# Optimization experiments

Hardware: AMD Instinct MI355X
Metric: run time of the kernel (lower is better)

Reference implementation:

```python
import jax, jax.numpy as jnp
import numpy as np
from jax import lax

NPOINT = 2048
RADIUS = 0.1
NSAMPLE = 32


def setup_inputs() -> dict:
    key = jax.random.key(0)
    ks = jax.random.split(key, 6)
    B, N, C = 8, 16384, 16
    xyz = jax.random.uniform(ks[0], (B, N, 3), dtype=jnp.float32)
    features = jax.random.normal(ks[1], (B, N, C), dtype=jnp.float32)
    W1 = jax.random.normal(ks[2], (C, 32), dtype=jnp.float32) * 0.1
    b1 = jnp.zeros((32,), jnp.float32)
    W2 = jax.random.normal(ks[3], (32, 32), dtype=jnp.float32) * 0.1
    b2 = jnp.zeros((32,), jnp.float32)
    W3 = jax.random.normal(ks[4], (32, 64), dtype=jnp.float32) * 0.1
    b3 = jnp.zeros((64,), jnp.float32)
    return {"xyz": xyz, "features": features,
            "W1": W1, "b1": b1, "W2": W2, "b2": b2, "W3": W3, "b3": b3}


def farthest_point_sample(xyz, npoint):
    # Sequential FPS: keep running min-distance to selected set, argmax each step.
    B, N, _ = xyz.shape

    def step(carry, _):
        min_d, far = carry  # min_d: [B,N], far: [B]
        centroid = jnp.take_along_axis(xyz, far[:, None, None], axis=1)  # [B,1,3]
        d = jnp.sum((xyz - centroid) ** 2, axis=-1)                      # [B,N]
        min_d = jnp.minimum(min_d, d)
        nxt = jnp.argmax(min_d, axis=1).astype(jnp.int32)
        return (min_d, nxt), far

    init = (jnp.full((B, N), 1e10, xyz.dtype), jnp.zeros((B,), jnp.int32))
    _, idx = lax.scan(step, init, None, length=npoint)  # idx: [npoint, B]
    return idx.T  # [B, npoint]


def ball_query(radius, nsample, xyz, new_xyz):
    # Squared pairwise distances [B, S, N]
    d2 = (jnp.sum(new_xyz ** 2, -1)[:, :, None]
          + jnp.sum(xyz ** 2, -1)[:, None, :]
          - 2.0 * jnp.einsum('bsd,bnd->bsn', new_xyz, xyz))
    N = xyz.shape[1]
    # Take the first `nsample` in-ball indices (by point order), pad with first found.
    scores = jnp.where(d2 <= radius * radius,
                       jnp.arange(N, dtype=jnp.int32), jnp.int32(N))
    vals = -lax.top_k(-scores, nsample)[0]  # smallest nsample scores, ascending
    first = vals[..., :1]                   # center itself is always in-ball
    return jnp.where(vals == N, first, vals)  # [B, S, nsample] int32


def reference(xyz, features, W1, b1, W2, b2, W3, b3):
    fps_idx = farthest_point_sample(xyz, NPOINT)                      # [B,S]
    new_xyz = jnp.take_along_axis(xyz, fps_idx[..., None], axis=1)    # [B,S,3]
    idx = ball_query(RADIUS, NSAMPLE, xyz, new_xyz)                   # [B,S,K]
    grouped = jax.vmap(lambda f, i: f[i])(features, idx)              # [B,S,K,C]
    h = jax.nn.relu(grouped @ W1 + b1)
    h = jax.nn.relu(h @ W2 + b2)
    h = h @ W3 + b3                                                   # [B,S,K,64]
    new_features = jnp.max(h, axis=2)                                 # [B,S,64]
    return new_xyz, new_features
```

## Files before the change

kernel.cpp:

```cpp
#include <hip/hip_runtime.h>

#define B 8
#define N 16384
#define S 2048
#define NS 32
#define CIN 16
#define NCELL 512

template<int CTRL>
__device__ __forceinline__ float dpp_fmax(float x) {
    int t = __builtin_amdgcn_update_dpp(0, __float_as_int(x), CTRL, 0xF, 0xF, true);
    return fmaxf(x, __int_as_float(t));
}
template<int CTRL>
__device__ __forceinline__ unsigned dpp_umax(unsigned x) {
    unsigned t = (unsigned)__builtin_amdgcn_update_dpp(0, (int)x, CTRL, 0xF, 0xF, true);
    return x > t ? x : t;
}
__device__ __forceinline__ float wave_fmax(float x) {
    x = dpp_fmax<0xB1>(x);
    x = dpp_fmax<0x4E>(x);
    x = dpp_fmax<0x114>(x);
    x = dpp_fmax<0x118>(x);
    x = dpp_fmax<0x142>(x);
    x = dpp_fmax<0x143>(x);
    return __int_as_float(__builtin_amdgcn_readlane(__float_as_int(x), 63));
}
__device__ __forceinline__ unsigned wave_umax(unsigned x) {
    x = dpp_umax<0xB1>(x);
    x = dpp_umax<0x4E>(x);
    x = dpp_umax<0x114>(x);
    x = dpp_umax<0x118>(x);
    x = dpp_umax<0x142>(x);
    x = dpp_umax<0x143>(x);
    return (unsigned)__builtin_amdgcn_readlane((int)x, 63);
}

__device__ __forceinline__ int expand3(int v) {
    return (v & 1) | ((v & 2) << 2) | ((v & 4) << 4);
}

__global__ __launch_bounds__(1024) void bucket_kernel(const float* __restrict__ xyz,
                                                      float* __restrict__ Xp,
                                                      float* __restrict__ Yp,
                                                      float* __restrict__ Zp,
                                                      int* __restrict__ Ip) {
    const int b = blockIdx.x;
    const int t = threadIdx.x;
    const float* xb = xyz + (size_t)b * N * 3;

    __shared__ int hist[NCELL], pA[NCELL], pB[NCELL], run[NCELL];
    if (t < NCELL) { hist[t] = 0; run[t] = 0; }
    __syncthreads();

    int cell[16];
    float xs[16], ys[16], zs[16];
#pragma unroll
    for (int k = 0; k < 16; ++k) {
        const int n = t + (k << 10);
        const float x = xb[3 * n + 0];
        const float y = xb[3 * n + 1];
        const float z = xb[3 * n + 2];
        int cx = min(7, max(0, (int)(x * 8.0f)));
        int cy = min(7, max(0, (int)(y * 8.0f)));
        int cz = min(7, max(0, (int)(z * 8.0f)));
        const int c = expand3(cx) | (expand3(cy) << 1) | (expand3(cz) << 2);
        cell[k] = c; xs[k] = x; ys[k] = y; zs[k] = z;
        atomicAdd(&hist[c], 1);
    }
    __syncthreads();

    int* cur = pA; int* nxt = pB;
    if (t < NCELL) cur[t] = hist[t];
    __syncthreads();
    for (int off = 1; off < NCELL; off <<= 1) {
        if (t < NCELL) nxt[t] = cur[t] + ((t >= off) ? cur[t - off] : 0);
        __syncthreads();
        int* tmp = cur; cur = nxt; nxt = tmp;
    }
    if (t < NCELL) nxt[t] = cur[t] - hist[t];
    __syncthreads();
    const int* base = nxt;

#pragma unroll
    for (int k = 0; k < 16; ++k) {
        const int c = cell[k];
        const int pos = base[c] + atomicAdd(&run[c], 1);
        const size_t o = (size_t)b * N + pos;
        Xp[o] = xs[k]; Yp[o] = ys[k]; Zp[o] = zs[k];
        Ip[o] = t + (k << 10);
    }
}

__global__ __launch_bounds__(1024, 1) void fps_prune_kernel(const float* __restrict__ xyz,
                                                            const float* __restrict__ Xp,
                                                            const float* __restrict__ Yp,
                                                            const float* __restrict__ Zp,
                                                            const int* __restrict__ Ip,
                                                            float* __restrict__ new_xyz) {
#pragma clang fp contract(off)
    const int b = blockIdx.x;
    const int t = threadIdx.x;
    const float* xb = xyz + (size_t)b * N * 3;
    const size_t base = (size_t)b * N + ((size_t)t << 4);

    float px[16], py[16], pz[16], md[16];
    int ip[16];
#pragma unroll
    for (int k = 0; k < 16; ++k) {
        px[k] = Xp[base + k];
        py[k] = Yp[base + k];
        pz[k] = Zp[base + k];
        ip[k] = Ip[base + k];
        md[k] = 1e10f;
    }
#pragma unroll
    for (int k = 0; k < 16; ++k) {
        asm volatile("" : "+v"(px[k]), "+v"(py[k]), "+v"(pz[k]), "+v"(ip[k]));
    }

    float lox = px[0], hix = px[0], loy = py[0], hiy = py[0], loz = pz[0], hiz = pz[0];
#pragma unroll
    for (int k = 1; k < 16; ++k) {
        lox = fminf(lox, px[k]); hix = fmaxf(hix, px[k]);
        loy = fminf(loy, py[k]); hiy = fmaxf(hiy, py[k]);
        loz = fminf(loz, pz[k]); hiz = fmaxf(hiz, pz[k]);
    }

    __shared__ unsigned long long slot3[3];
    if (t == 0) { slot3[0] = 0ull; slot3[1] = 0ull; slot3[2] = 0ull; }
    __syncthreads();

    int far = 0;
    int p = 0;
    float ub = 1e10f;
    int cand = ip[0];

    for (int it = 0; it < S; ++it) {
        const float cx = xb[3 * far + 0];
        const float cy = xb[3 * far + 1];
        const float cz = xb[3 * far + 2];
        if (t == 0) {
            float* o = new_xyz + ((size_t)b * S + it) * 3;
            o[0] = cx; o[1] = cy; o[2] = cz;
        }
        const float ddx = fmaxf(0.0f, fmaxf(lox - cx, cx - hix));
        const float ddy = fmaxf(0.0f, fmaxf(loy - cy, cy - hiy));
        const float ddz = fmaxf(0.0f, fmaxf(loz - cz, cz - hiz));
        const float lb = (ddx * ddx + ddy * ddy) + ddz * ddz;

        if (!(lb * 0.99998f > ub)) {
            float nu = 0.0f;
#pragma unroll
            for (int k = 0; k < 16; ++k) {
                const float dx = __fsub_rn(px[k], cx);
                const float dy = __fsub_rn(py[k], cy);
                const float dz = __fsub_rn(pz[k], cz);
                const float d  = __fadd_rn(__fadd_rn(__fmul_rn(dx, dx), __fmul_rn(dy, dy)),
                                           __fmul_rn(dz, dz));
                const float m = fminf(md[k], d);
                md[k] = m;
                nu = fmaxf(nu, m);
            }
            int c = 0x7fffffff;
#pragma unroll
            for (int k = 0; k < 16; ++k) {
                if (md[k] == nu) c = min(c, ip[k]);
            }
            ub = nu; cand = c;
        }
        const float wmax = wave_fmax(ub);
        unsigned cn = (ub == wmax) ? ~(unsigned)cand : 0u;
        cn = wave_umax(cn);
        if ((t & 63) == 0) {
            atomicMax(&slot3[p],
                      ((unsigned long long)__float_as_uint(wmax) << 32) | (unsigned long long)cn);
        }
        int pn = p + 1; if (pn == 3) pn = 0;
        if (t == 0) slot3[pn] = 0ull;
        __syncthreads();
        const unsigned long long r = slot3[p];
        far = (int)(~(unsigned)r);
        p = pn;
    }
}

__global__ __launch_bounds__(1024) void fps_kernel(const float* __restrict__ xyz,
                                                   float* __restrict__ new_xyz) {
#pragma clang fp contract(off)
    const int b = blockIdx.x;
    const int t = threadIdx.x;
    const float* xb = xyz + (size_t)b * N * 3;

    float px[16], py[16], pz[16], md[16];
#pragma unroll
    for (int k = 0; k < 16; ++k) {
        const int n = t + (k << 10);
        px[k] = xb[3 * n + 0];
        py[k] = xb[3 * n + 1];
        pz[k] = xb[3 * n + 2];
        md[k] = 1e10f;
    }
    __shared__ float rv[2][16];
    __shared__ int slot[2];
    if (t == 0) { slot[0] = 0x7fffffff; slot[1] = 0x7fffffff; }
    __syncthreads();
    int far = 0, p = 0;
    const int lane = t & 63, w = t >> 6;
    for (int it = 0; it < S; ++it) {
        const float cx = xb[3 * far + 0], cy = xb[3 * far + 1], cz = xb[3 * far + 2];
        if (t == 0) {
            float* o = new_xyz + ((size_t)b * S + it) * 3;
            o[0] = cx; o[1] = cy; o[2] = cz;
        }
        float bestv = -1.0f;
#pragma unroll
        for (int k = 0; k < 16; ++k) {
            const float dx = __fsub_rn(px[k], cx);
            const float dy = __fsub_rn(py[k], cy);
            const float dz = __fsub_rn(pz[k], cz);
            const float d  = __fadd_rn(__fadd_rn(__fmul_rn(dx, dx), __fmul_rn(dy, dy)),
                                       __fmul_rn(dz, dz));
            const float m = fminf(md[k], d);
            md[k] = m;
            bestv = fmaxf(bestv, m);
        }
        float v = bestv;
#pragma unroll
        for (int off = 32; off >= 1; off >>= 1) v = fmaxf(v, __shfl_xor(v, off));
        if (lane == 0) rv[p][w] = v;
        __syncthreads();
        float u = rv[p][lane & 15];
#pragma unroll
        for (int off = 8; off >= 1; off >>= 1) u = fmaxf(u, __shfl_xor(u, off));
        if (t == 0) slot[p ^ 1] = 0x7fffffff;
        if (bestv == u) {
            int cnd2 = 0x7fffffff;
#pragma unroll
            for (int k = 0; k < 16; ++k)
                if (md[k] == u) cnd2 = min(cnd2, t + (k << 10));
            atomicMin(&slot[p], cnd2);
        }
        __syncthreads();
        far = slot[p];
        p ^= 1;
    }
}

__global__ __launch_bounds__(64) void ball_mlp_kernel(
    const float* __restrict__ xyz,
    const float* __restrict__ feat,
    const float* __restrict__ W1, const float* __restrict__ b1,
    const float* __restrict__ W2, const float* __restrict__ b2,
    const float* __restrict__ W3, const float* __restrict__ b3,
    const float* __restrict__ new_xyz,
    float* __restrict__ out_feat) {
#pragma clang fp contract(off)
    const int q = blockIdx.x;
    const int b = q >> 11;
    const int lane = threadIdx.x;
    const float* xb = xyz + (size_t)b * N * 3;

    const double qx = (double)new_xyz[3 * q + 0];
    const double qy = (double)new_xyz[3 * q + 1];
    const double qz = (double)new_xyz[3 * q + 2];
    const double s2 = qx * qx + qy * qy + qz * qz;
    const double R2 = 0.1 * 0.1;

    __shared__ int idxbuf[NS];
    int found = 0;
    for (int bs = 0; bs < N; bs += 64) {
        const int n = bs + lane;
        const double x = (double)xb[3 * n + 0];
        const double y = (double)xb[3 * n + 1];
        const double z = (double)xb[3 * n + 2];
        const double n2 = x * x + y * y + z * z;
        const double dt = qx * x + qy * y + qz * z;
        const double d2 = (s2 + n2) - 2.0 * dt;
        const bool ok = (d2 <= R2);
        const unsigned long long msk = __ballot(ok);
        if (ok) {
            const int pos = found + (int)__popcll(msk & ((1ull << lane) - 1ull));
            if (pos < NS) idxbuf[pos] = n;
        }
        found += (int)__popcll(msk);
        if (found >= NS) break;
    }
    __syncthreads();
    if (lane == 0) {
        const int cnt = found < NS ? found : NS;
        const int first = (cnt > 0) ? idxbuf[0] : (N - 1);
        for (int j2 = cnt; j2 < NS; ++j2) idxbuf[j2] = first;
    }
    __syncthreads();

    const int j = lane & 31;
    const int h = lane >> 5;
    const int nid = idxbuf[j];
    const float* fp = feat + ((size_t)b * N + nid) * CIN;
    float fv[CIN];
#pragma unroll
    for (int k = 0; k < CIN; ++k) fv[k] = fp[k];

    float h1[32];
#pragma unroll
    for (int c = 0; c < 32; ++c) {
        float a = b1[c];
#pragma unroll
        for (int k = 0; k < CIN; ++k) a = fmaf(fv[k], W1[(k << 5) + c], a);
        h1[c] = fmaxf(a, 0.0f);
    }
    float h2[32];
#pragma unroll
    for (int c = 0; c < 32; ++c) {
        float a = b2[c];
#pragma unroll
        for (int k = 0; k < 32; ++k) a = fmaf(h1[k], W2[(k << 5) + c], a);
        h2[c] = fmaxf(a, 0.0f);
    }
    const int cbase = h << 5;
    float mx[32];
#pragma unroll
    for (int c = 0; c < 32; ++c) {
        float a = b3[cbase + c];
#pragma unroll
        for (int k = 0; k < 32; ++k) a = fmaf(h2[k], W3[(k << 6) + cbase + c], a);
        mx[c] = a;
    }
#pragma unroll
    for (int off = 1; off <= 16; off <<= 1) {
#pragma unroll
        for (int c = 0; c < 32; ++c) mx[c] = fmaxf(mx[c], __shfl_xor(mx[c], off));
    }
    if (j == 0) {
        float* o = out_feat + (size_t)q * 64 + cbase;
#pragma unroll
        for (int c = 0; c < 32; ++c) o[c] = mx[c];
    }
}

extern "C" void kernel_launch(void* const* d_in, const int* in_sizes, int n_in,
                              void* d_out, int out_size, void* d_ws, size_t ws_size,
                              hipStream_t stream) {
    (void)in_sizes; (void)n_in; (void)out_size;
    const float* xyz  = (const float*)d_in[0];
    const float* feat = (const float*)d_in[1];
    const float* W1   = (const float*)d_in[2];
    const float* b1   = (const float*)d_in[3];
    const float* W2   = (const float*)d_in[4];
    const float* b2   = (const float*)d_in[5];
    const float* W3   = (const float*)d_in[6];
    const float* b3   = (const float*)d_in[7];

    float* out      = (float*)d_out;
    float* new_xyz  = out;
    float* new_feat = out + (size_t)B * S * 3;

    const size_t need = (size_t)4 * B * N * sizeof(float);
    if (ws_size >= need) {
        float* Xp = (float*)d_ws;
        float* Yp = Xp + (size_t)B * N;
        float* Zp = Yp + (size_t)B * N;
        int*   Ip = (int*)(Zp + (size_t)B * N);
        bucket_kernel<<<B, 1024, 0, stream>>>(xyz, Xp, Yp, Zp, Ip);
        fps_prune_kernel<<<B, 1024, 0, stream>>>(xyz, Xp, Yp, Zp, Ip, new_xyz);
    } else {
        fps_kernel<<<B, 1024, 0, stream>>>(xyz, new_xyz);
    }
    ball_mlp_kernel<<<B * S, 64, 0, stream>>>(xyz, feat, W1, b1, W2, b2, W3, b3,
                                              new_xyz, new_feat);
}
```

Before: 2.413 ms.

## Vectorize pruned FPS distances with packed float2 and skip idle-wave reductions

The pruned FPS kernel now holds each thread's points as float2 vectors, so loads are 64-bit and the distance arithmetic can use packed FP32 instructions. When no lane in a wave needs an update, the wave skips both the distance recompute and the DPP wave reductions and reuses its previous max key. The next centroid's coordinates are loaded right after the barrier instead of at the top of the loop. The risks are that packed operations may not match the original rounding with contraction off, and that the cached wave key relies on the per-wave bound never changing when the wave is idle.

```diff
diff --git a/kernel.cpp b/kernel.cpp
--- a/kernel.cpp
+++ b/kernel.cpp
@@ -6,6 +6,9 @@
 #define NS 32
 #define CIN 16
 #define NCELL 512
+
+typedef float f32x2 __attribute__((ext_vector_type(2)));
+typedef int   i32x2 __attribute__((ext_vector_type(2)));
 
 template<int CTRL>
 __device__ __forceinline__ float dpp_fmax(float x) {
@@ -104,42 +107,40 @@
     const float* xb = xyz + (size_t)b * N * 3;
     const size_t base = (size_t)b * N + ((size_t)t << 4);
 
-    float px[16], py[16], pz[16], md[16];
-    int ip[16];
-#pragma unroll
-    for (int k = 0; k < 16; ++k) {
-        px[k] = Xp[base + k];
-        py[k] = Yp[base + k];
-        pz[k] = Zp[base + k];
-        ip[k] = Ip[base + k];
-        md[k] = 1e10f;
-    }
-#pragma unroll
-    for (int k = 0; k < 16; ++k) {
-        asm volatile("" : "+v"(px[k]), "+v"(py[k]), "+v"(pz[k]), "+v"(ip[k]));
-    }
-
-    float lox = px[0], hix = px[0], loy = py[0], hiy = py[0], loz = pz[0], hiz = pz[0];
-#pragma unroll
-    for (int k = 1; k < 16; ++k) {
-        lox = fminf(lox, px[k]); hix = fmaxf(hix, px[k]);
-        loy = fminf(loy, py[k]); hiy = fmaxf(hiy, py[k]);
-        loz = fminf(loz, pz[k]); hiz = fmaxf(hiz, pz[k]);
+    f32x2 px[8], py[8], pz[8], md[8];
+    i32x2 ip[8];
+    {
+        const f32x2* X2 = (const f32x2*)(Xp + base);
+        const f32x2* Y2 = (const f32x2*)(Yp + base);
+        const f32x2* Z2 = (const f32x2*)(Zp + base);
+        const i32x2* I2 = (const i32x2*)(Ip + base);
+#pragma unroll
+        for (int j = 0; j < 8; ++j) {
+            px[j] = X2[j]; py[j] = Y2[j]; pz[j] = Z2[j]; ip[j] = I2[j];
+            md[j] = (f32x2){1e10f, 1e10f};
+        }
+    }
+
+    float lox = px[0].x, hix = px[0].x, loy = py[0].x, hiy = py[0].x,
+          loz = pz[0].x, hiz = pz[0].x;
+#pragma unroll
+    for (int j = 0; j < 8; ++j) {
+        lox = fminf(lox, fminf(px[j].x, px[j].y)); hix = fmaxf(hix, fmaxf(px[j].x, px[j].y));
+        loy = fminf(loy, fminf(py[j].x, py[j].y)); hiy = fmaxf(hiy, fmaxf(py[j].x, py[j].y));
+        loz = fminf(loz, fminf(pz[j].x, pz[j].y)); hiz = fmaxf(hiz, fmaxf(pz[j].x, pz[j].y));
     }
 
     __shared__ unsigned long long slot3[3];
     if (t == 0) { slot3[0] = 0ull; slot3[1] = 0ull; slot3[2] = 0ull; }
     __syncthreads();
 
-    int far = 0;
     int p = 0;
     float ub = 1e10f;
-    int cand = ip[0];
+    int cand = ip[0].x;
+    unsigned long long wkey = 0ull;
+    float cx = xb[0], cy = xb[1], cz = xb[2];
 
     for (int it = 0; it < S; ++it) {
-        const float cx = xb[3 * far + 0];
-        const float cy = xb[3 * far + 1];
-        const float cz = xb[3 * far + 2];
         if (t == 0) {
             float* o = new_xyz + ((size_t)b * S + it) * 3;
             o[0] = cx; o[1] = cy; o[2] = cz;
@@ -148,39 +149,59 @@
         const float ddy = fmaxf(0.0f, fmaxf(loy - cy, cy - hiy));
         const float ddz = fmaxf(0.0f, fmaxf(loz - cz, cz - hiz));
         const float lb = (ddx * ddx + ddy * ddy) + ddz * ddz;
-
-        if (!(lb * 0.99998f > ub)) {
-            float nu = 0.0f;
-#pragma unroll
-            for (int k = 0; k < 16; ++k) {
-                const float dx = __fsub_rn(px[k], cx);
-                const float dy = __fsub_rn(py[k], cy);
-                const float dz = __fsub_rn(pz[k], cz);
-                const float d  = __fadd_rn(__fadd_rn(__fmul_rn(dx, dx), __fmul_rn(dy, dy)),
-                                           __fmul_rn(dz, dz));
-                const float m = fminf(md[k], d);
-                md[k] = m;
-                nu = fmaxf(nu, m);
+        const bool upd = !(lb * 0.99998f > ub);
+
+        if (__any(upd)) {
+            if (upd) {
+                asm volatile("" : "+v"(px[0]), "+v"(px[1]), "+v"(px[2]), "+v"(px[3]),
+                                  "+v"(px[4]), "+v"(px[5]), "+v"(px[6]), "+v"(px[7]));
+                asm volatile("" : "+v"(py[0]), "+v"(py[1]), "+v"(py[2]), "+v"(py[3]),
+                                  "+v"(py[4]), "+v"(py[5]), "+v"(py[6]), "+v"(py[7]));
+                asm volatile("" : "+v"(pz[0]), "+v"(pz[1]), "+v"(pz[2]), "+v"(pz[3]),
+                                  "+v"(pz[4]), "+v"(pz[5]), "+v"(pz[6]), "+v"(pz[7]));
+                asm volatile("" : "+v"(ip[0]), "+v"(ip[1]), "+v"(ip[2]), "+v"(ip[3]),
+                                  "+v"(ip[4]), "+v"(ip[5]), "+v"(ip[6]), "+v"(ip[7]));
+                const f32x2 c2x = {cx, cx}, c2y = {cy, cy}, c2z = {cz, cz};
+                float nu = 0.0f;
+#pragma unroll
+                for (int j = 0; j < 8; ++j) {
+                    const f32x2 dx = px[j] - c2x;
+                    const f32x2 dy = py[j] - c2y;
+                    const f32x2 dz = pz[j] - c2z;
+                    const f32x2 xx = dx * dx;
+                    const f32x2 yy = dy * dy;
+                    const f32x2 zz = dz * dz;
+                    const f32x2 ss = xx + yy;
+                    const f32x2 dd = ss + zz;
+                    f32x2 m;
+                    m.x = fminf(md[j].x, dd.x);
+                    m.y = fminf(md[j].y, dd.y);
+                    md[j] = m;
+                    nu = fmaxf(nu, fmaxf(m.x, m.y));
+                }
+                int c = 0x7fffffff;
+#pragma unroll
+                for (int j = 0; j < 8; ++j) {
+                    if (md[j].x == nu) c = min(c, ip[j].x);
+                    if (md[j].y == nu) c = min(c, ip[j].y);
+                }
+                ub = nu; cand = c;
             }
-            int c = 0x7fffffff;
-#pragma unroll
-            for (int k = 0; k < 16; ++k) {
-                if (md[k] == nu) c = min(c, ip[k]);
-            }
-            ub = nu; cand = c;
-        }
-        const float wmax = wave_fmax(ub);
-        unsigned cn = (ub == wmax) ? ~(unsigned)cand : 0u;
-        cn = wave_umax(cn);
-        if ((t & 63) == 0) {
-            atomicMax(&slot3[p],
-                      ((unsigned long long)__float_as_uint(wmax) << 32) | (unsigned long long)cn);
-        }
+            const float wmax = wave_fmax(ub);
+            unsigned cn = (ub == wmax) ? ~(unsigned)cand : 0u;
+            cn = wave_umax(cn);
+            wkey = ((unsigned long long)__float_as_uint(wmax) << 32)
+                 | (unsigned long long)cn;
+        }
+        if ((t & 63) == 0) atomicMax(&slot3[p], wkey);
         int pn = p + 1; if (pn == 3) pn = 0;
         if (t == 0) slot3[pn] = 0ull;
         __syncthreads();
         const unsigned long long r = slot3[p];
-        far = (int)(~(unsigned)r);
+        const int far = (int)(~(unsigned)r);
+        cx = xb[3 * far + 0];
+        cy = xb[3 * far + 1];
+        cz = xb[3 * far + 2];
         p = pn;
     }
 }
```

Measured after the change: 2.362 ms. 1.02x faster.
